# Optimization experiments

Hardware: AMD Instinct MI355X
Metric: run time of the kernel (lower is better)

Reference implementation:

```python
import jax, jax.numpy as jnp
import numpy as np

C_IN = 64
C_QK = C_IN // 8  # 8
B, H, W = 8, 64, 64


def setup_inputs() -> dict:
    key = jax.random.key(0)
    ks = jax.random.split(key, 8)
    s_in = 1.0 / np.sqrt(C_IN)
    return {
        "x": jax.random.normal(ks[0], (B, C_IN, H, W), dtype=jnp.float32),
        "Wf": jax.random.normal(ks[1], (C_QK, C_IN), dtype=jnp.float32) * s_in,
        "bf": jax.random.normal(ks[2], (C_QK,), dtype=jnp.float32) * 0.01,
        "Wg": jax.random.normal(ks[3], (C_QK, C_IN), dtype=jnp.float32) * s_in,
        "bg": jax.random.normal(ks[4], (C_QK,), dtype=jnp.float32) * 0.01,
        "Wh": jax.random.normal(ks[5], (C_IN, C_IN), dtype=jnp.float32) * s_in,
        "bh": jax.random.normal(ks[6], (C_IN,), dtype=jnp.float32) * 0.01,
        "gamma": jax.random.normal(ks[7], (1,), dtype=jnp.float32) * 0.1,
    }


def reference(x, Wf, bf, Wg, bg, Wh, bh, gamma):
    Bn, C, Hn, Wn = x.shape
    N = Hn * Wn
    xf = x.reshape(Bn, C, N)  # (B, C, HW)
    # 1x1 convs == per-pixel linear projections
    fx = jnp.einsum('bcn,oc->bno', xf, Wf) + bf            # (B, HW, C/8)  (permuted query)
    gx = jnp.einsum('bcn,oc->bon', xf, Wg) + bg[:, None]   # (B, C/8, HW)
    hx = jnp.einsum('bcn,oc->bon', xf, Wh) + bh[:, None]   # (B, C,  HW)
    s_mtx = jnp.einsum('bno,bom->bnm', fx, gx)             # (B, HW, HW)
    attention = jax.nn.softmax(s_mtx, axis=-2)             # softmax over dim=-2 (rows)
    o = jnp.einsum('bcn,bnm->bcm', hx, attention)          # (B, C, HW)
    return x + gamma * o.reshape(Bn, C, Hn, Wn)
```

## Files before the change

kernel.cpp:

```cpp
#include <hip/hip_runtime.h>
#include <hip/hip_bf16.h>
#include <math.h>

#define CIN 64
#define CQK 8
#define BATCH 8
#define NPOS 4096
#define TN 128
#define NT (NPOS / TN)

typedef __attribute__((ext_vector_type(8))) short s16x8;
typedef __attribute__((ext_vector_type(4))) float f32x4;
typedef __attribute__((ext_vector_type(16))) float f32x16;

#define Z16 {0,0,0,0,0,0,0,0,0,0,0,0,0,0,0,0}

__device__ inline unsigned cvt_pk_bf16(float lo, float hi) {
    unsigned r;
    asm("v_cvt_pk_bf16_f32 %0, %1, %2" : "=v"(r) : "v"(lo), "v"(hi));
    return r;
}

__global__ __launch_bounds__(256) void proj_kernel(
    const float* __restrict__ x,
    const float* __restrict__ Wf, const float* __restrict__ bf,
    const float* __restrict__ Wg, const float* __restrict__ bg,
    const float* __restrict__ Wh, const float* __restrict__ bh,
    unsigned short* __restrict__ Kp, unsigned short* __restrict__ Qp,
    unsigned short* __restrict__ Vimg)
{
    __shared__ float xs[CIN * 34];
    __shared__ float bss[80];

    const int tid = threadIdx.x;
    const int b   = blockIdx.y;
    const int n0  = blockIdx.x * 32;

    if (tid < 80)
        bss[tid] = (tid < 8) ? bf[tid] : (tid < 16) ? bg[tid - 8] : bh[tid - 16];

    {
        const int c   = tid >> 2;
        const int seg = tid & 3;
        const float* src = x + ((size_t)(b * CIN + c)) * NPOS + n0 + seg * 8;
        float* dst = xs + c * 34 + seg * 8;
#pragma unroll
        for (int k = 0; k < 2; ++k) {
            const float4 v = *(const float4*)(src + k * 4);
            *(float2*)(dst + k * 4)     = make_float2(v.x, v.y);
            *(float2*)(dst + k * 4 + 2) = make_float2(v.z, v.w);
        }
    }

    const int l    = tid & 63;
    const int w    = tid >> 6;
    const int ng   = w >> 1;
    const int role = w & 1;
    const int lm   = l & 15;
    const int h    = l >> 4;

    auto wfrag = [&](const float* Wrow) -> s16x8 {
        const float4 a  = *(const float4*)(Wrow);
        const float4 bq = *(const float4*)(Wrow + 4);
        union { unsigned u[4]; s16x8 v; } r;
        r.u[0] = cvt_pk_bf16(a.x, a.y);
        r.u[1] = cvt_pk_bf16(a.z, a.w);
        r.u[2] = cvt_pk_bf16(bq.x, bq.y);
        r.u[3] = cvt_pk_bf16(bq.z, bq.w);
        return r.v;
    };

    s16x8 wkq0 = {0,0,0,0,0,0,0,0}, wkq1 = {0,0,0,0,0,0,0,0};
    if (role == 0) {
        const float* kqrow = (lm < 8) ? (Wf + lm * CIN) : (Wg + (lm - 8) * CIN);
        wkq0 = wfrag(kqrow + h * 8);
        wkq1 = wfrag(kqrow + h * 8 + 32);
    }
    s16x8 wv0[2], wv1[2];
#pragma unroll
    for (int vt = 0; vt < 2; ++vt) {
        const float* vr = Wh + ((role * 2 + vt) * 16 + lm) * CIN + h * 8;
        wv0[vt] = wfrag(vr);
        wv1[vt] = wfrag(vr + 32);
    }

    __syncthreads();

    union { unsigned u[4]; s16x8 v; } xf0, xf1;
#pragma unroll
    for (int e2 = 0; e2 < 4; ++e2) {
        const int c = h * 8 + e2 * 2;
        xf0.u[e2] = cvt_pk_bf16(xs[c * 34 + ng * 16 + lm],
                                xs[(c + 1) * 34 + ng * 16 + lm]);
        xf1.u[e2] = cvt_pk_bf16(xs[(c + 32) * 34 + ng * 16 + lm],
                                xs[(c + 33) * 34 + ng * 16 + lm]);
    }

    const f32x4 z = {0.f, 0.f, 0.f, 0.f};
    f32x4 va[2];
#pragma unroll
    for (int vt = 0; vt < 2; ++vt) {
        va[vt] = __builtin_amdgcn_mfma_f32_16x16x32_bf16(xf0.v, wv0[vt], z, 0, 0, 0);
        va[vt] = __builtin_amdgcn_mfma_f32_16x16x32_bf16(xf1.v, wv1[vt], va[vt], 0, 0, 0);
    }

    const float LOG2E = 1.44269504088896f;

    if (role == 0) {
        f32x4 kq = __builtin_amdgcn_mfma_f32_16x16x32_bf16(wkq0, xf0.v, z, 0, 0, 0);
        kq = __builtin_amdgcn_mfma_f32_16x16x32_bf16(wkq1, xf1.v, kq, 0, 0, 0);
        const int n = n0 + ng * 16 + lm;
        float v0 = kq[0] + bss[h * 4 + 0];
        float v1 = kq[1] + bss[h * 4 + 1];
        float v2 = kq[2] + bss[h * 4 + 2];
        float v3 = kq[3] + bss[h * 4 + 3];
        if (h >= 2) { v0 *= LOG2E; v1 *= LOG2E; v2 *= LOG2E; v3 *= LOG2E; }
        uint2 pk;
        pk.x = cvt_pk_bf16(v0, v1);
        pk.y = cvt_pk_bf16(v2, v3);
        unsigned short* dstq =
            (h < 2 ? Kp : Qp) + ((size_t)(b * NPOS + n)) * CQK + (h & 1) * 4;
        *(uint2*)dstq = pk;
    }

    {
        const int t128 = n0 >> 7;
        const int sub  = (n0 & 127) >> 5;
        unsigned short* dstB =
            Vimg + ((size_t)(b * 32 + t128)) * 8192 + (size_t)sub * 2048;
        const int jj   = (h & 1) * 2 + ng;
        const int half = h >> 1;
#pragma unroll
        for (int vt = 0; vt < 2; ++vt) {
            const int C = (role * 2 + vt) * 16 + lm;
            const float bb = bss[16 + C];
            uint2 pk;
            pk.x = cvt_pk_bf16(va[vt][0] + bb, va[vt][1] + bb);
            pk.y = cvt_pk_bf16(va[vt][2] + bb, va[vt][3] + bb);
            const int p = ((jj & 1) * 2 + (C >> 5)) * 64 + (jj >> 1) * 32 + (C & 31);
            *(uint2*)(dstB + p * 8 + half * 4) = pk;
        }
    }
}

__global__ __launch_bounds__(256, 3) void attn_kernel(
    const unsigned short* __restrict__ Kp, const unsigned short* __restrict__ Qp,
    const unsigned short* __restrict__ Vimg, const float* __restrict__ x,
    const float* __restrict__ gamma, float* __restrict__ out)
{
    __shared__ __align__(16) float smem[4 * 64 * 36 + 256];
    float* reg = smem;
    float* rsl = smem + 4 * 64 * 36;

    const int tid = threadIdx.x;
    const int l   = tid & 63;
    const int w   = tid >> 6;
    const int lc  = l & 31;
    const int h   = l >> 5;
    const int id  = blockIdx.x;
    const int b   = id & 7;
    const int m0  = (id >> 3) * 64;

    const unsigned short* Kbat = Kp + (size_t)b * NPOS * CQK;
    const char* Vbat = (const char*)(Vimg + (size_t)b * NPOS * CIN);

    s16x8 qf0 = {0,0,0,0,0,0,0,0}, qf1 = {0,0,0,0,0,0,0,0};
    if (h == 0) {
        qf0 = *(const s16x8*)(Qp + ((size_t)(b * NPOS + m0 + lc)) * CQK);
        qf1 = *(const s16x8*)(Qp + ((size_t)(b * NPOS + m0 + 32 + lc)) * CQK);
    }

    f32x16 acc00 = Z16, acc01 = Z16, acc10 = Z16, acc11 = Z16;
    float rsum0 = 0.f, rsum1 = 0.f;

    s16x8 vfA[4], vfB[4], ka0, ka1;
    f32x16 sc0, sc1;
    const f32x16 z = Z16;

    auto loadV = [&](s16x8* vf, int t) {
        const char* base = Vbat + (size_t)t * 16384 + w * 4096 + l * 16;
#pragma unroll
        for (int c = 0; c < 4; ++c)
            vf[c] = *(const s16x8*)(base + c * 1024);
    };
    auto loadK = [&](s16x8& kr, int t) {
        kr = *(const s16x8*)(Kbat + ((size_t)(t * TN + w * 32 + lc)) * CQK);
    };

    auto slot = [&](s16x8* vfCur, const s16x8& kaUse, s16x8& kaLd,
                    int t, int doNext) {
        if (doNext) asm volatile("s_waitcnt vmcnt(4)" ::: "memory");
        else        asm volatile("s_waitcnt vmcnt(0)" ::: "memory");
        __builtin_amdgcn_s_setprio(1);
#pragma unroll
        for (int rr = 0; rr < 16; ++rr) {
            sc0[rr] = __builtin_amdgcn_exp2f(sc0[rr]);
            sc1[rr] = __builtin_amdgcn_exp2f(sc1[rr]);
        }
        union { unsigned u[4]; s16x8 v; } A1, A2, B1, B2;
#pragma unroll
        for (int i = 0; i < 4; ++i) {
            A1.u[i] = cvt_pk_bf16(sc0[2 * i], sc0[2 * i + 1]);
            A2.u[i] = cvt_pk_bf16(sc0[8 + 2 * i], sc0[9 + 2 * i]);
            B1.u[i] = cvt_pk_bf16(sc1[2 * i], sc1[2 * i + 1]);
            B2.u[i] = cvt_pk_bf16(sc1[8 + 2 * i], sc1[9 + 2 * i]);
        }
        rsum0 += (((sc0[0] + sc0[1]) + (sc0[2] + sc0[3])) +
                  ((sc0[4] + sc0[5]) + (sc0[6] + sc0[7]))) +
                 (((sc0[8] + sc0[9]) + (sc0[10] + sc0[11])) +
                  ((sc0[12] + sc0[13]) + (sc0[14] + sc0[15])));
        rsum1 += (((sc1[0] + sc1[1]) + (sc1[2] + sc1[3])) +
                  ((sc1[4] + sc1[5]) + (sc1[6] + sc1[7]))) +
                 (((sc1[8] + sc1[9]) + (sc1[10] + sc1[11])) +
                  ((sc1[12] + sc1[13]) + (sc1[14] + sc1[15])));
        if (doNext) {
            sc0 = __builtin_amdgcn_mfma_f32_32x32x16_bf16(kaUse, qf0, z, 0, 0, 0);
            sc1 = __builtin_amdgcn_mfma_f32_32x32x16_bf16(kaUse, qf1, z, 0, 0, 0);
            int tl = t + 2; if (tl > NT - 1) tl = NT - 1;
            loadK(kaLd, tl);
        }
        acc00 = __builtin_amdgcn_mfma_f32_32x32x16_bf16(A1.v, vfCur[0], acc00, 0, 0, 0);
        acc00 = __builtin_amdgcn_mfma_f32_32x32x16_bf16(A2.v, vfCur[2], acc00, 0, 0, 0);
        acc01 = __builtin_amdgcn_mfma_f32_32x32x16_bf16(A1.v, vfCur[1], acc01, 0, 0, 0);
        acc01 = __builtin_amdgcn_mfma_f32_32x32x16_bf16(A2.v, vfCur[3], acc01, 0, 0, 0);
        acc10 = __builtin_amdgcn_mfma_f32_32x32x16_bf16(B1.v, vfCur[0], acc10, 0, 0, 0);
        acc10 = __builtin_amdgcn_mfma_f32_32x32x16_bf16(B2.v, vfCur[2], acc10, 0, 0, 0);
        acc11 = __builtin_amdgcn_mfma_f32_32x32x16_bf16(B1.v, vfCur[1], acc11, 0, 0, 0);
        acc11 = __builtin_amdgcn_mfma_f32_32x32x16_bf16(B2.v, vfCur[3], acc11, 0, 0, 0);
        __builtin_amdgcn_s_setprio(0);
        if (doNext) {
            int tl = t + 2; if (tl > NT - 1) tl = NT - 1;
            loadV(vfCur, tl);
        }
    };

    loadK(ka0, 0); loadV(vfA, 0);
    loadK(ka1, 1); loadV(vfB, 1);
    asm volatile("s_waitcnt vmcnt(9)" ::: "memory");
    sc0 = __builtin_amdgcn_mfma_f32_32x32x16_bf16(ka0, qf0, z, 0, 0, 0);
    sc1 = __builtin_amdgcn_mfma_f32_32x32x16_bf16(ka0, qf1, z, 0, 0, 0);

    slot(vfA, ka1, ka0, 0, 1);
#pragma unroll 1
    for (int i = 0; i < 15; ++i) {
        const int t = 1 + 2 * i;
        slot(vfB, ka0, ka1, t, 1);
        slot(vfA, ka1, ka0, t + 1, 1);
    }
    slot(vfB, ka0, ka1, 31, 0);

    rsum0 += __shfl_xor(rsum0, 32, 64);
    rsum1 += __shfl_xor(rsum1, 32, 64);
    if (h == 0) {
        rsl[w * 64 + lc]      = rsum0;
        rsl[w * 64 + 32 + lc] = rsum1;
    }

    const float gm = gamma[0];
    auto epi = [&](const f32x16& a0, const f32x16& a1, int mOff) {
#pragma unroll
        for (int rq = 0; rq < 4; ++rq) {
            const int mb = 8 * rq + 4 * h;
            const f32x4 q0 = {a0[4 * rq], a0[4 * rq + 1], a0[4 * rq + 2], a0[4 * rq + 3]};
            const f32x4 q1 = {a1[4 * rq], a1[4 * rq + 1], a1[4 * rq + 2], a1[4 * rq + 3]};
            *(f32x4*)(reg + w * 2304 + lc * 36 + mb)        = q0;
            *(f32x4*)(reg + w * 2304 + (32 + lc) * 36 + mb) = q1;
        }
        __syncthreads();
        const int c  = tid >> 2;
        const int mq = tid & 3;
        const size_t base = ((size_t)(b * CIN + c)) * NPOS + m0 + mOff + mq * 8;
#pragma unroll
        for (int q4 = 0; q4 < 2; ++q4) {
            const float4 xv = *(const float4*)(x + base + q4 * 4);
            float4 o;
#pragma unroll
            for (int i = 0; i < 4; ++i) {
                const int ml = mq * 8 + q4 * 4 + i;
                const float rsum = (rsl[mOff + ml] + rsl[64 + mOff + ml]) +
                                   (rsl[128 + mOff + ml] + rsl[192 + mOff + ml]);
                const int oi = c * 36 + ml;
                const float os = (reg[oi] + reg[2304 + oi]) + (reg[4608 + oi] + reg[6912 + oi]);
                ((float*)&o)[i] = ((const float*)&xv)[i] + gm * os / rsum;
            }
            *(float4*)(out + base + q4 * 4) = o;
        }
        __syncthreads();
    };
    epi(acc00, acc01, 0);
    epi(acc10, acc11, 32);
}

extern "C" void kernel_launch(void* const* d_in, const int* in_sizes, int n_in,
                              void* d_out, int out_size, void* d_ws, size_t ws_size,
                              hipStream_t stream) {
    const float* x     = (const float*)d_in[0];
    const float* Wf    = (const float*)d_in[1];
    const float* bf    = (const float*)d_in[2];
    const float* Wg    = (const float*)d_in[3];
    const float* bg    = (const float*)d_in[4];
    const float* Wh    = (const float*)d_in[5];
    const float* bh    = (const float*)d_in[6];
    const float* gamma = (const float*)d_in[7];
    float* out = (float*)d_out;

    unsigned short* Kp   = (unsigned short*)d_ws;
    unsigned short* Qp   = Kp + (size_t)BATCH * NPOS * CQK;
    unsigned short* Vimg = Qp + (size_t)BATCH * NPOS * CQK;

    dim3 pgrid(NPOS / 32, BATCH);
    proj_kernel<<<pgrid, 256, 0, stream>>>(x, Wf, bf, Wg, bg, Wh, bh, Kp, Qp, Vimg);

    attn_kernel<<<dim3(BATCH * NPOS / 64), 256, 0, stream>>>(Kp, Qp, Vimg, x, gamma, out);
}
```

Baseline: 44.83 us.

## Replace exp2 with Schraudolph bit-trick exp and compute row sums via MFMA

Q is prescaled by log2e·2^23 and the score MFMA accumulates from a constant bias of 127·2^23, so converting each score to int and reinterpreting the bits as float gives a piecewise-linear exp2 with no transcendental instructions. Row sums of the softmax denominator move from scalar adds to extra MFMAs against a ones vector. Occupancy hint drops from 3 to 2 blocks to fit the additional accumulator registers. This trades accuracy of the exponential (Schraudolph approximation, with no max subtraction) and extra matrix work for removing the VALU exp and reduction cost.

```diff
diff --git a/kernel.cpp b/kernel.cpp
--- a/kernel.cpp
+++ b/kernel.cpp
@@ -15,10 +15,15 @@
 
 #define Z16 {0,0,0,0,0,0,0,0,0,0,0,0,0,0,0,0}
 
+#define SCH_BIAS 1065353216.0f
+
 __device__ inline unsigned cvt_pk_bf16(float lo, float hi) {
     unsigned r;
     asm("v_cvt_pk_bf16_f32 %0, %1, %2" : "=v"(r) : "v"(lo), "v"(hi));
     return r;
+}
+__device__ inline float sch_exp(float y) {
+    return __builtin_bit_cast(float, (int)y);
 }
 
 __global__ __launch_bounds__(256) void proj_kernel(
@@ -104,7 +109,7 @@
         va[vt] = __builtin_amdgcn_mfma_f32_16x16x32_bf16(xf1.v, wv1[vt], va[vt], 0, 0, 0);
     }
 
-    const float LOG2E = 1.44269504088896f;
+    const float QSCALE = 1.44269504088896f * 8388608.0f;
 
     if (role == 0) {
         f32x4 kq = __builtin_amdgcn_mfma_f32_16x16x32_bf16(wkq0, xf0.v, z, 0, 0, 0);
@@ -114,7 +119,7 @@
         float v1 = kq[1] + bss[h * 4 + 1];
         float v2 = kq[2] + bss[h * 4 + 2];
         float v3 = kq[3] + bss[h * 4 + 3];
-        if (h >= 2) { v0 *= LOG2E; v1 *= LOG2E; v2 *= LOG2E; v3 *= LOG2E; }
+        if (h >= 2) { v0 *= QSCALE; v1 *= QSCALE; v2 *= QSCALE; v3 *= QSCALE; }
         uint2 pk;
         pk.x = cvt_pk_bf16(v0, v1);
         pk.y = cvt_pk_bf16(v2, v3);
@@ -143,7 +148,7 @@
     }
 }
 
-__global__ __launch_bounds__(256, 3) void attn_kernel(
+__global__ __launch_bounds__(256, 2) void attn_kernel(
     const unsigned short* __restrict__ Kp, const unsigned short* __restrict__ Qp,
     const unsigned short* __restrict__ Vimg, const float* __restrict__ x,
     const float* __restrict__ gamma, float* __restrict__ out)
@@ -171,11 +176,16 @@
     }
 
     f32x16 acc00 = Z16, acc01 = Z16, acc10 = Z16, acc11 = Z16;
-    float rsum0 = 0.f, rsum1 = 0.f;
+    f32x16 rs0 = Z16, rs1 = Z16;
+    const s16x8 vones = {0x3F80, 0x3F80, 0x3F80, 0x3F80,
+                         0x3F80, 0x3F80, 0x3F80, 0x3F80};
+    const f32x16 bias16 = {SCH_BIAS, SCH_BIAS, SCH_BIAS, SCH_BIAS,
+                           SCH_BIAS, SCH_BIAS, SCH_BIAS, SCH_BIAS,
+                           SCH_BIAS, SCH_BIAS, SCH_BIAS, SCH_BIAS,
+                           SCH_BIAS, SCH_BIAS, SCH_BIAS, SCH_BIAS};
 
     s16x8 vfA[4], vfB[4], ka0, ka1;
     f32x16 sc0, sc1;
-    const f32x16 z = Z16;
 
     auto loadV = [&](s16x8* vf, int t) {
         const char* base = Vbat + (size_t)t * 16384 + w * 4096 + l * 16;
@@ -192,33 +202,24 @@
         if (doNext) asm volatile("s_waitcnt vmcnt(4)" ::: "memory");
         else        asm volatile("s_waitcnt vmcnt(0)" ::: "memory");
         __builtin_amdgcn_s_setprio(1);
-#pragma unroll
-        for (int rr = 0; rr < 16; ++rr) {
-            sc0[rr] = __builtin_amdgcn_exp2f(sc0[rr]);
-            sc1[rr] = __builtin_amdgcn_exp2f(sc1[rr]);
-        }
         union { unsigned u[4]; s16x8 v; } A1, A2, B1, B2;
 #pragma unroll
         for (int i = 0; i < 4; ++i) {
-            A1.u[i] = cvt_pk_bf16(sc0[2 * i], sc0[2 * i + 1]);
-            A2.u[i] = cvt_pk_bf16(sc0[8 + 2 * i], sc0[9 + 2 * i]);
-            B1.u[i] = cvt_pk_bf16(sc1[2 * i], sc1[2 * i + 1]);
-            B2.u[i] = cvt_pk_bf16(sc1[8 + 2 * i], sc1[9 + 2 * i]);
-        }
-        rsum0 += (((sc0[0] + sc0[1]) + (sc0[2] + sc0[3])) +
-                  ((sc0[4] + sc0[5]) + (sc0[6] + sc0[7]))) +
-                 (((sc0[8] + sc0[9]) + (sc0[10] + sc0[11])) +
-                  ((sc0[12] + sc0[13]) + (sc0[14] + sc0[15])));
-        rsum1 += (((sc1[0] + sc1[1]) + (sc1[2] + sc1[3])) +
-                  ((sc1[4] + sc1[5]) + (sc1[6] + sc1[7]))) +
-                 (((sc1[8] + sc1[9]) + (sc1[10] + sc1[11])) +
-                  ((sc1[12] + sc1[13]) + (sc1[14] + sc1[15])));
+            A1.u[i] = cvt_pk_bf16(sch_exp(sc0[2 * i]),     sch_exp(sc0[2 * i + 1]));
+            A2.u[i] = cvt_pk_bf16(sch_exp(sc0[8 + 2 * i]), sch_exp(sc0[9 + 2 * i]));
+            B1.u[i] = cvt_pk_bf16(sch_exp(sc1[2 * i]),     sch_exp(sc1[2 * i + 1]));
+            B2.u[i] = cvt_pk_bf16(sch_exp(sc1[8 + 2 * i]), sch_exp(sc1[9 + 2 * i]));
+        }
         if (doNext) {
-            sc0 = __builtin_amdgcn_mfma_f32_32x32x16_bf16(kaUse, qf0, z, 0, 0, 0);
-            sc1 = __builtin_amdgcn_mfma_f32_32x32x16_bf16(kaUse, qf1, z, 0, 0, 0);
+            sc0 = __builtin_amdgcn_mfma_f32_32x32x16_bf16(kaUse, qf0, bias16, 0, 0, 0);
+            sc1 = __builtin_amdgcn_mfma_f32_32x32x16_bf16(kaUse, qf1, bias16, 0, 0, 0);
             int tl = t + 2; if (tl > NT - 1) tl = NT - 1;
             loadK(kaLd, tl);
         }
+        rs0 = __builtin_amdgcn_mfma_f32_32x32x16_bf16(A1.v, vones, rs0, 0, 0, 0);
+        rs0 = __builtin_amdgcn_mfma_f32_32x32x16_bf16(A2.v, vones, rs0, 0, 0, 0);
+        rs1 = __builtin_amdgcn_mfma_f32_32x32x16_bf16(B1.v, vones, rs1, 0, 0, 0);
+        rs1 = __builtin_amdgcn_mfma_f32_32x32x16_bf16(B2.v, vones, rs1, 0, 0, 0);
         acc00 = __builtin_amdgcn_mfma_f32_32x32x16_bf16(A1.v, vfCur[0], acc00, 0, 0, 0);
         acc00 = __builtin_amdgcn_mfma_f32_32x32x16_bf16(A2.v, vfCur[2], acc00, 0, 0, 0);
         acc01 = __builtin_amdgcn_mfma_f32_32x32x16_bf16(A1.v, vfCur[1], acc01, 0, 0, 0);
@@ -237,8 +238,8 @@
     loadK(ka0, 0); loadV(vfA, 0);
     loadK(ka1, 1); loadV(vfB, 1);
     asm volatile("s_waitcnt vmcnt(9)" ::: "memory");
-    sc0 = __builtin_amdgcn_mfma_f32_32x32x16_bf16(ka0, qf0, z, 0, 0, 0);
-    sc1 = __builtin_amdgcn_mfma_f32_32x32x16_bf16(ka0, qf1, z, 0, 0, 0);
+    sc0 = __builtin_amdgcn_mfma_f32_32x32x16_bf16(ka0, qf0, bias16, 0, 0, 0);
+    sc1 = __builtin_amdgcn_mfma_f32_32x32x16_bf16(ka0, qf1, bias16, 0, 0, 0);
 
     slot(vfA, ka1, ka0, 0, 1);
 #pragma unroll 1
@@ -249,11 +250,15 @@
     }
     slot(vfB, ka0, ka1, 31, 0);
 
-    rsum0 += __shfl_xor(rsum0, 32, 64);
-    rsum1 += __shfl_xor(rsum1, 32, 64);
-    if (h == 0) {
-        rsl[w * 64 + lc]      = rsum0;
-        rsl[w * 64 + 32 + lc] = rsum1;
+    if (lc == 0) {
+#pragma unroll
+        for (int rq = 0; rq < 4; ++rq) {
+            const int mb = 8 * rq + 4 * h;
+            const f32x4 r0 = {rs0[4 * rq], rs0[4 * rq + 1], rs0[4 * rq + 2], rs0[4 * rq + 3]};
+            const f32x4 r1 = {rs1[4 * rq], rs1[4 * rq + 1], rs1[4 * rq + 2], rs1[4 * rq + 3]};
+            *(f32x4*)(rsl + w * 64 + mb)      = r0;
+            *(f32x4*)(rsl + w * 64 + 32 + mb) = r1;
+        }
     }
 
     const float gm = gamma[0];
```

New measurement: 40.73 us. 1.1x faster.
